# Kernel optimization log

Hardware: AMD Instinct MI355X
Metric: run time of the kernel (lower is better)

## Reference

```python
import jax, jax.numpy as jnp
import numpy as np

# Config constants (match init_kwargs)
T = 1024            # num_tokens
H = 2048            # hidden_size
E = 16              # n_routed_experts
I = 1408            # moe_intermediate_size
TOP_K = 4           # num_experts_per_tok
N_GROUP = 4         # n_group
TOPK_GROUP = 2      # topk_group
N_SHARED = 2        # n_shared_experts
SI = I * N_SHARED   # shared intermediate = 2816
ROUTED_SCALE = 1.0  # routed_scaling_factor
RENORMALIZE = True  # norm_topk_prob


def setup_inputs() -> dict:
    key = jax.random.key(0)
    ks = jax.random.split(key, 6)
    scale_w = 0.02  # keep router logits in a sane range
    return {
        "x": jax.random.normal(ks[0], (T, H), dtype=jnp.float32),
        "gate_w": jax.random.normal(ks[1], (E, H), dtype=jnp.float32) * scale_w,
        "w_gate_up": jax.random.normal(ks[2], (E, H, 2 * I), dtype=jnp.float32) * scale_w,
        "w_down": jax.random.normal(ks[3], (E, I, H), dtype=jnp.float32) * scale_w,
        "shared_gate_up": jax.random.normal(ks[4], (H, 2 * SI), dtype=jnp.float32) * scale_w,
        "shared_down": jax.random.normal(ks[5], (SI, H), dtype=jnp.float32) * scale_w,
    }


def _silu_and_mul(gu):
    gate, up = jnp.split(gu, 2, axis=-1)
    return jax.nn.silu(gate) * up


def _grouped_topk(logits):
    # scores over experts, grouped top-k group selection, then top-k experts
    scores = jax.nn.softmax(logits, axis=-1)                          # [T, E]
    group_scores = scores.reshape(T, N_GROUP, E // N_GROUP).max(-1)   # [T, G]
    _, grp_idx = jax.lax.top_k(group_scores, TOPK_GROUP)              # [T, topk_group]
    grp_mask = jnp.zeros((T, N_GROUP), scores.dtype).at[
        jnp.arange(T)[:, None], grp_idx].set(1.0)                     # [T, G]
    score_mask = jnp.repeat(grp_mask, E // N_GROUP, axis=1)           # [T, E]
    tmp = jnp.where(score_mask > 0, scores, 0.0)
    topk_w, topk_ids = jax.lax.top_k(tmp, TOP_K)                      # [T, K]
    if RENORMALIZE:
        topk_w = topk_w / jnp.sum(topk_w, axis=-1, keepdims=True)
    # dense combine-weight matrix [T, E] (top-k ids are distinct per token)
    cw = jnp.zeros((T, E), scores.dtype).at[
        jnp.arange(T)[:, None], topk_ids].set(topk_w)
    return cw


def reference(x, gate_w, w_gate_up, w_down, shared_gate_up, shared_down):
    # shared experts MLP (SiluAndMul)
    shared_out = _silu_and_mul(x @ shared_gate_up) @ shared_down      # [T, H]

    # router
    logits = x @ gate_w.T                                             # [T, E]
    cw = _grouped_topk(logits)                                        # [T, E]

    # routed experts: dense grouped GEMM over all experts, masked combine
    h = jnp.einsum('th,ehi->eti', x, w_gate_up)                       # [E, T, 2I]
    a = _silu_and_mul(h)                                              # [E, T, I]
    y = jnp.einsum('eti,eih->eth', a, w_down)                         # [E, T, H]
    routed = jnp.einsum('eth,te->th', y, cw)                          # [T, H]

    return routed * ROUTED_SCALE + shared_out
```

## Files before the change

kernel.cpp:

```cpp
#include <hip/hip_runtime.h>
#include <hip/hip_bf16.h>
#include <stdint.h>
#include <math.h>

#define T_TOK 1024
#define H_DIM 2048
#define E_NUM 16
#define I_DIM 1408
#define TOPK  4
#define SI_DIM 2816
#define NSLOT (T_TOK * TOPK)

typedef short bf16x8 __attribute__((ext_vector_type(8)));
typedef float f32x4  __attribute__((ext_vector_type(4)));

__device__ __forceinline__ uint32_t fbf(float f) {
  __hip_bfloat16 h = __float2bfloat16(f);
  return (uint32_t)*reinterpret_cast<uint16_t*>(&h);
}
__device__ __forceinline__ float asf(uint32_t u) {
  union { uint32_t u; float f; } c; c.u = u; return c.f;
}

typedef const __attribute__((address_space(1))) char gld_g;
typedef __attribute__((address_space(3))) char gld_l;
__device__ __forceinline__ void gload16(const void* g, void* l) {
  __builtin_amdgcn_global_load_lds((gld_g*)g, (gld_l*)l, 16, 0, 0);
}
__device__ __forceinline__ void barrier_lgkm() {
  asm volatile("s_waitcnt lgkmcnt(0)" ::: "memory");
  __builtin_amdgcn_s_barrier();
  __builtin_amdgcn_sched_barrier(0);
}

__global__ __launch_bounds__(256) void k_router(const float* __restrict__ x,
                                                const float* __restrict__ gw,
                                                int* __restrict__ topk_id,
                                                float* __restrict__ topk_w) {
  int t = blockIdx.x;
  float acc[E_NUM];
#pragma unroll
  for (int e = 0; e < E_NUM; ++e) acc[e] = 0.f;
  for (int h = threadIdx.x; h < H_DIM; h += 256) {
    float xv = x[(long)t * H_DIM + h];
#pragma unroll
    for (int e = 0; e < E_NUM; ++e) acc[e] += xv * gw[e * H_DIM + h];
  }
#pragma unroll
  for (int e = 0; e < E_NUM; ++e) {
#pragma unroll
    for (int off = 32; off; off >>= 1) acc[e] += __shfl_down(acc[e], off);
  }
  __shared__ float part[4][E_NUM];
  int wid = threadIdx.x >> 6, lane = threadIdx.x & 63;
  if (lane == 0) {
#pragma unroll
    for (int e = 0; e < E_NUM; ++e) part[wid][e] = acc[e];
  }
  __syncthreads();
  if (threadIdx.x == 0) {
    float lg[E_NUM], p[E_NUM];
    float m = -1e30f;
    for (int e = 0; e < E_NUM; ++e) {
      lg[e] = part[0][e] + part[1][e] + part[2][e] + part[3][e];
      m = fmaxf(m, lg[e]);
    }
    float s = 0.f;
    for (int e = 0; e < E_NUM; ++e) { p[e] = expf(lg[e] - m); s += p[e]; }
    float inv = 1.f / s;
    for (int e = 0; e < E_NUM; ++e) p[e] *= inv;
    float gs[4];
    for (int g = 0; g < 4; ++g) {
      float mg = p[g * 4];
      for (int i = 1; i < 4; ++i) mg = fmaxf(mg, p[g * 4 + i]);
      gs[g] = mg;
    }
    int g1 = 0;
    for (int g = 1; g < 4; ++g) if (gs[g] > gs[g1]) g1 = g;
    int g2 = -1;
    for (int g = 0; g < 4; ++g) {
      if (g == g1) continue;
      if (g2 < 0 || gs[g] > gs[g2]) g2 = g;
    }
    float q[E_NUM];
    for (int e = 0; e < E_NUM; ++e)
      q[e] = ((e >> 2) == g1 || (e >> 2) == g2) ? p[e] : -1e30f;
    int ids[TOPK]; float wv[TOPK]; float wsum = 0.f;
    for (int k = 0; k < TOPK; ++k) {
      int best = 0; float bv = -2e30f;
      for (int e = 0; e < E_NUM; ++e) if (q[e] > bv) { bv = q[e]; best = e; }
      ids[k] = best; wv[k] = p[best]; wsum += p[best]; q[best] = -3e30f;
    }
    float winv = 1.f / wsum;
    for (int k = 0; k < TOPK; ++k) {
      topk_id[t * TOPK + k] = ids[k];
      topk_w[t * TOPK + k] = wv[k] * winv;
    }
  }
}

__global__ __launch_bounds__(256) void k_count(const int* __restrict__ topk_id,
                                               int* __restrict__ counts) {
  int e = blockIdx.x, tid = threadIdx.x;
  int c = 0;
  for (int s = tid; s < NSLOT; s += 256) c += (topk_id[s] == e);
#pragma unroll
  for (int off = 32; off; off >>= 1) c += __shfl_down(c, off);
  __shared__ int wsum[4];
  int wid = tid >> 6, lane = tid & 63;
  if (lane == 0) wsum[wid] = c;
  __syncthreads();
  if (tid == 0) counts[e] = wsum[0] + wsum[1] + wsum[2] + wsum[3];
}

__global__ void k_offs(const int* __restrict__ counts, int* __restrict__ offs,
                       int* __restrict__ cum) {
  if (threadIdx.x == 0 && blockIdx.x == 0) {
    int s = 0, c = 0;
    cum[0] = 0;
    for (int e = 0; e < E_NUM; ++e) {
      offs[e] = s; s += counts[e];
      c += (counts[e] + 255) >> 8;
      cum[e + 1] = c;
    }
    offs[E_NUM] = s;
  }
}

__global__ __launch_bounds__(256) void k_fill(const int* __restrict__ topk_id,
                                              const int* __restrict__ offs,
                                              int* __restrict__ tok_of_row,
                                              int* __restrict__ row_of_slot) {
  int e = blockIdx.x, tid = threadIdx.x;
  int t0 = tid * 4;
  int match[4]; int cnt = 0;
#pragma unroll
  for (int i = 0; i < 4; ++i) {
    int t = t0 + i; int mk = -1;
#pragma unroll
    for (int k = 0; k < TOPK; ++k) if (topk_id[t * TOPK + k] == e) mk = k;
    match[i] = mk; cnt += (mk >= 0);
  }
  __shared__ int sc[256];
  sc[tid] = cnt; __syncthreads();
  for (int d = 1; d < 256; d <<= 1) {
    int v = sc[tid];
    if (tid >= d) v += sc[tid - d];
    __syncthreads();
    sc[tid] = v;
    __syncthreads();
  }
  int row = offs[e] + sc[tid] - cnt;
#pragma unroll
  for (int i = 0; i < 4; ++i) {
    if (match[i] >= 0) {
      tok_of_row[row] = t0 + i;
      row_of_slot[(t0 + i) * TOPK + match[i]] = row;
      ++row;
    }
  }
}

__global__ __launch_bounds__(256) void k_cvt(const float* __restrict__ in,
                                             uint16_t* __restrict__ out) {
  int i = (blockIdx.x * 256 + threadIdx.x) * 4;
  float4 v = *(const float4*)(in + i);
  uint2 p;
  p.x = fbf(v.x) | (fbf(v.y) << 16);
  p.y = fbf(v.z) | (fbf(v.w) << 16);
  *(uint2*)(out + i) = p;
}

template <int MODE>
__global__ __launch_bounds__(256, 2) void k_gemm(
    const uint16_t* __restrict__ As, int ldas,
    const float* __restrict__ Bs, int ldbs, int upS,
    void* __restrict__ OutS, int ldoS, int NMs, int NNs, int Ks, int f32S,
    const uint16_t* __restrict__ Ar, int ldar,
    const float* __restrict__ Br, int ldbr, long bstr, int upR,
    void* __restrict__ OutR, int ldoR, int NN1, int K1, int f32R,
    const int* __restrict__ offs, const int* __restrict__ rowlist,
    const int* __restrict__ cum) {
  constexpr int BN = (MODE == 0) ? 64 : 128;
  constexpr int NI = (MODE == 0) ? 2 : 4;
  constexpr int BB = 32768;
  constexpr int BMS = 5120;
  __shared__ char smem[43008];

  const int S = NMs * NNs;
  const int NBw = S + cum[E_NUM] * NN1;
  int f = blockIdx.x;
  if (f >= NBw) return;
  int q = NBw >> 3, r = NBw & 7;
  int xcd = f & 7, o = f >> 3;
  int f2 = (xcd < r ? xcd * (q + 1) : r * (q + 1) + (xcd - r) * q) + o;

  const uint16_t* A; const float* Bp; void* Outp; const int* rl;
  int lda, ldb, up, ldo, K, m0, n0, row_end, isf32;
  if (f2 < S) {
    int mb = f2 % NMs, nb = f2 / NMs;
    A = As; lda = ldas; Bp = Bs; ldb = ldbs; up = upS;
    Outp = OutS; ldo = ldoS; K = Ks; isf32 = f32S; rl = nullptr;
    m0 = mb * 256; row_end = NMs * 256; n0 = nb * BN;
  } else {
    int g = f2 - S;
    int e = 0;
    for (e = 0; e < E_NUM; ++e) if (g < cum[e + 1] * NN1) break;
    if (e == E_NUM) return;
    int nmbe = cum[e + 1] - cum[e];
    int loc = g - cum[e] * NN1;
    int mb = loc % nmbe, nb = loc / nmbe;
    A = Ar; lda = ldar; Bp = Br + (size_t)e * bstr; ldb = ldbr; up = upR;
    Outp = OutR; ldo = ldoR; K = K1; isf32 = f32R; rl = rowlist;
    m0 = offs[e] + mb * 256; row_end = offs[e + 1]; n0 = nb * BN;
  }

  const int tid = threadIdx.x;
  const int wid = tid >> 6, lane = tid & 63;
  const int wm = (wid >> 1) * 64, wn = (wid & 1) * (BN / 2);
  const int lrow = lane & 15, kg = lane >> 4;

  const uint16_t* aSrc[4]; int aDst[4];
#pragma unroll
  for (int p = 0; p < 4; ++p) {
    int rr = wid * 64 + p * 16 + (lane >> 2);
    int grow = m0 + rr;
    grow = grow < row_end - 1 ? grow : row_end - 1;
    int arow = rl ? rl[grow] : grow;
    int sslot = (lane & 3) ^ ((lane >> 3) & 3);
    aSrc[p] = A + (size_t)arow * lda + sslot * 8;
    aDst[p] = wid * 4096 + p * 1024;
  }

  int n4, kq, mat;
  if constexpr (MODE == 0) {
    n4 = (tid & 15) * 4; int rest = tid >> 4; kq = rest & 7; mat = rest >> 3;
  } else {
    n4 = (tid & 31) * 4; kq = tid >> 5; mat = 0;
  }
  const int k0 = kq * 4;
  const float* bptr = Bp + (size_t)k0 * ldb + n0 + n4 + (mat ? up : 0);
  const int sq = (kq >> 1) & 3, hf = kq & 1;
  int bw[4];
#pragma unroll
  for (int j = 0; j < 4; ++j) {
    int n = n4 + j;
    bw[j] = BB + mat * BMS + n * 80 + ((sq ^ ((n >> 4) & 3)) << 4) + (hf << 3);
  }

  float4 v[4];
  auto loadB = [&]() {
#pragma unroll
    for (int i = 0; i < 4; ++i) v[i] = *(const float4*)(bptr + (size_t)i * ldb);
    bptr += (size_t)32 * ldb;
  };
  auto stageB = [&]() {
#pragma unroll
    for (int j = 0; j < 4; ++j) {
      uint2 w;
      w.x = fbf(((const float*)&v[0])[j]) | (fbf(((const float*)&v[1])[j]) << 16);
      w.y = fbf(((const float*)&v[2])[j]) | (fbf(((const float*)&v[3])[j]) << 16);
      *(uint2*)(smem + bw[j]) = w;
    }
  };

  f32x4 zero = {0.f, 0.f, 0.f, 0.f};
  f32x4 accg[2][4][NI];
  f32x4 accu[(MODE == 0) ? 2 : 1][(MODE == 0) ? 4 : 1][(MODE == 0) ? NI : 1];
#pragma unroll
  for (int mt = 0; mt < 2; ++mt)
#pragma unroll
    for (int mi = 0; mi < 4; ++mi)
#pragma unroll
      for (int ni = 0; ni < NI; ++ni) {
        accg[mt][mi][ni] = zero;
        if constexpr (MODE == 0) accu[mt][mi][ni] = zero;
      }

  auto compute = [&](int cur) {
    const char* ab = smem + cur * 16384;
    const int akx = (kg ^ ((lrow >> 1) & 3)) << 4;
    bf16x8 af[8];
#pragma unroll
    for (int mt = 0; mt < 2; ++mt)
#pragma unroll
      for (int mi = 0; mi < 4; ++mi) {
        int row = mt * 128 + wm + mi * 16 + lrow;
        af[mt * 4 + mi] = *(const bf16x8*)(ab + row * 64 + akx);
      }
#pragma unroll
    for (int ni = 0; ni < NI; ++ni) {
      int n = wn + ni * 16 + lrow;
      int bo = BB + n * 80 + ((kg ^ ((n >> 4) & 3)) << 4);
      bf16x8 bg = *(const bf16x8*)(smem + bo);
#pragma unroll
      for (int mt = 0; mt < 2; ++mt)
#pragma unroll
        for (int mi = 0; mi < 4; ++mi)
          accg[mt][mi][ni] = __builtin_amdgcn_mfma_f32_16x16x32_bf16(
              af[mt * 4 + mi], bg, accg[mt][mi][ni], 0, 0, 0);
      if constexpr (MODE == 0) {
        bf16x8 bu = *(const bf16x8*)(smem + bo + BMS);
#pragma unroll
        for (int mt = 0; mt < 2; ++mt)
#pragma unroll
          for (int mi = 0; mi < 4; ++mi)
            accu[mt][mi][ni] = __builtin_amdgcn_mfma_f32_16x16x32_bf16(
                af[mt * 4 + mi], bu, accu[mt][mi][ni], 0, 0, 0);
      }
    }
  };

  const int nk = K >> 5;
#pragma unroll
  for (int p = 0; p < 4; ++p) { gload16(aSrc[p], smem + aDst[p]); aSrc[p] += 32; }
  loadB();

  for (int kt = 0; kt < nk; ++kt) {
    const int cur = kt & 1;
    __syncthreads();
    if (kt + 1 < nk) {
#pragma unroll
      for (int p = 0; p < 4; ++p) {
        gload16(aSrc[p], smem + (cur ^ 1) * 16384 + aDst[p]); aSrc[p] += 32;
      }
    }
    stageB();
    if (kt + 1 < nk) loadB();
    barrier_lgkm();
    compute(cur);
  }

#pragma unroll
  for (int mt = 0; mt < 2; ++mt) {
#pragma unroll
    for (int mi = 0; mi < 4; ++mi) {
#pragma unroll
      for (int rr = 0; rr < 4; ++rr) {
        int grow = m0 + mt * 128 + wm + mi * 16 + kg * 4 + rr;
        if (grow >= row_end) continue;
#pragma unroll
        for (int ni = 0; ni < NI; ++ni) {
          int col = n0 + wn + ni * 16 + lrow;
          float g = accg[mt][mi][ni][rr];
          if constexpr (MODE == 0) {
            float u = accu[mt][mi][ni][rr];
            float a = g / (1.f + __expf(-g)) * u;
            ((uint16_t*)Outp)[(size_t)grow * ldo + col] = (uint16_t)fbf(a);
          } else {
            if (isf32)
              ((float*)Outp)[(size_t)grow * ldo + col] = g;
            else
              ((uint16_t*)Outp)[(size_t)grow * ldo + col] = (uint16_t)fbf(g);
          }
        }
      }
    }
  }
}

__global__ __launch_bounds__(256) void k_combine(float* __restrict__ out,
    const uint16_t* __restrict__ y, const int* __restrict__ row_of_slot,
    const float* __restrict__ topk_w, const float* __restrict__ p0) {
  int t = blockIdx.x, tid = threadIdx.x;
  int h = tid * 8;
  size_t off = (size_t)t * H_DIM + h;
  float4 o0 = *(const float4*)(p0 + off);
  float4 o1 = *(const float4*)(p0 + off + 4);
#pragma unroll
  for (int k = 0; k < TOPK; ++k) {
    int row = row_of_slot[t * TOPK + k];
    float wk = topk_w[t * TOPK + k];
    uint4 v = *(const uint4*)(y + (size_t)row * H_DIM + h);
    o0.x += wk * asf(v.x << 16); o0.y += wk * asf(v.x & 0xffff0000u);
    o0.z += wk * asf(v.y << 16); o0.w += wk * asf(v.y & 0xffff0000u);
    o1.x += wk * asf(v.z << 16); o1.y += wk * asf(v.z & 0xffff0000u);
    o1.z += wk * asf(v.w << 16); o1.w += wk * asf(v.w & 0xffff0000u);
  }
  *(float4*)(out + off) = o0;
  *(float4*)(out + off + 4) = o1;
}

extern "C" void kernel_launch(void* const* d_in, const int* in_sizes, int n_in,
                              void* d_out, int out_size, void* d_ws,
                              size_t ws_size, hipStream_t stream) {
  const float* x   = (const float*)d_in[0];
  const float* gw  = (const float*)d_in[1];
  const float* wgu = (const float*)d_in[2];
  const float* wd  = (const float*)d_in[3];
  const float* sgu = (const float*)d_in[4];
  const float* sd  = (const float*)d_in[5];
  float* out = (float*)d_out;

  char* ws = (char*)d_ws;
  int*   topk_id     = (int*)(ws + 0);
  float* topk_w      = (float*)(ws + 16384);
  int*   counts      = (int*)(ws + 32768);
  int*   offs        = (int*)(ws + 33792);
  int*   cum         = (int*)(ws + 34816);
  int*   tok_of_row  = (int*)(ws + 35840);
  int*   row_of_slot = (int*)(ws + 52224);
  uint16_t* x_bf     = (uint16_t*)(ws + 131072);
  uint16_t* act      = (uint16_t*)(ws + 4325376);
  uint16_t* yslots   = (uint16_t*)(ws + 15859712);
  uint16_t* act_sh   = (uint16_t*)(ws + 32636928);
  bool merged = ws_size >= (size_t)38404096 + 8388608;
  float* p0 = merged ? (float*)(ws + 38404096) : (float*)(ws + 4325376);

  k_router<<<T_TOK, 256, 0, stream>>>(x, gw, topk_id, topk_w);
  k_count<<<E_NUM, 256, 0, stream>>>(topk_id, counts);
  k_offs<<<1, 1, 0, stream>>>(counts, offs, cum);
  k_fill<<<E_NUM, 256, 0, stream>>>(topk_id, offs, tok_of_row, row_of_slot);
  k_cvt<<<(T_TOK * H_DIM) / 1024, 256, 0, stream>>>(x, x_bf);

  k_gemm<0><<<176 + 32 * 22, 256, 0, stream>>>(
      x_bf, H_DIM, sgu, 2 * SI_DIM, SI_DIM, act_sh, SI_DIM, 4, 44, H_DIM, 0,
      x_bf, H_DIM, wgu, 2 * I_DIM, (long)H_DIM * 2 * I_DIM, I_DIM,
      act, I_DIM, 22, H_DIM, 0,
      offs, tok_of_row, cum);

  if (merged) {
    k_gemm<1><<<64 + 32 * 16, 256, 0, stream>>>(
        act_sh, SI_DIM, sd, H_DIM, 0, p0, H_DIM, 4, 16, SI_DIM, 1,
        act, I_DIM, wd, H_DIM, (long)I_DIM * H_DIM, 0,
        yslots, H_DIM, 16, I_DIM, 0,
        offs, nullptr, cum);
  } else {
    k_gemm<1><<<32 * 16, 256, 0, stream>>>(
        act_sh, SI_DIM, sd, H_DIM, 0, p0, H_DIM, 4, 0, SI_DIM, 1,
        act, I_DIM, wd, H_DIM, (long)I_DIM * H_DIM, 0,
        yslots, H_DIM, 16, I_DIM, 0,
        offs, nullptr, cum);
    k_gemm<1><<<64, 256, 0, stream>>>(
        act_sh, SI_DIM, sd, H_DIM, 0, p0, H_DIM, 4, 16, SI_DIM, 1,
        act, I_DIM, wd, H_DIM, (long)I_DIM * H_DIM, 0,
        yslots, H_DIM, 0, I_DIM, 0,
        offs, nullptr, cum);
  }
  k_combine<<<T_TOK, 256, 0, stream>>>(out, yslots, row_of_slot, topk_w, p0);
}
```

Baseline: 322.1 us.

## Stream fp32 B tiles directly into LDS and convert to bf16 at fragment read

Replaces the register-staged B path (global float4 loads, bf16 packing, LDS store) with asynchronous global_load_lds copies of raw fp32 B tiles into a double-buffered, XOR-swizzled LDS region. Each MFMA B fragment is now assembled from eight scalar fp32 LDS reads converted to bf16 inside the compute loop. The goal is to remove staging registers and the extra barrier so B loads overlap compute like the A loads already do. In exchange, LDS use grows to 64KB per block, LDS read traffic roughly doubles, and every wave repeats the fp32-to-bf16 conversion on the MFMA critical path.

```diff
diff --git a/kernel.cpp b/kernel.cpp
--- a/kernel.cpp
+++ b/kernel.cpp
@@ -26,11 +26,6 @@
 typedef __attribute__((address_space(3))) char gld_l;
 __device__ __forceinline__ void gload16(const void* g, void* l) {
   __builtin_amdgcn_global_load_lds((gld_g*)g, (gld_l*)l, 16, 0, 0);
-}
-__device__ __forceinline__ void barrier_lgkm() {
-  asm volatile("s_waitcnt lgkmcnt(0)" ::: "memory");
-  __builtin_amdgcn_s_barrier();
-  __builtin_amdgcn_sched_barrier(0);
 }
 
 __global__ __launch_bounds__(256) void k_router(const float* __restrict__ x,
@@ -183,9 +178,9 @@
     const int* __restrict__ cum) {
   constexpr int BN = (MODE == 0) ? 64 : 128;
   constexpr int NI = (MODE == 0) ? 2 : 4;
-  constexpr int BB = 32768;
-  constexpr int BMS = 5120;
-  __shared__ char smem[43008];
+  constexpr int ROWB = BN * 4;
+  constexpr int MATS = (MODE == 0) ? 8192 : 0;
+  __shared__ char smem[65536];
 
   const int S = NMs * NNs;
   const int NBw = S + cum[E_NUM] * NN1;
@@ -231,36 +226,39 @@
     aSrc[p] = A + (size_t)arow * lda + sslot * 8;
     aDst[p] = wid * 4096 + p * 1024;
   }
-
-  int n4, kq, mat;
-  if constexpr (MODE == 0) {
-    n4 = (tid & 15) * 4; int rest = tid >> 4; kq = rest & 7; mat = rest >> 3;
-  } else {
-    n4 = (tid & 31) * 4; kq = tid >> 5; mat = 0;
-  }
-  const int k0 = kq * 4;
-  const float* bptr = Bp + (size_t)k0 * ldb + n0 + n4 + (mat ? up : 0);
-  const int sq = (kq >> 1) & 3, hf = kq & 1;
-  int bw[4];
-#pragma unroll
-  for (int j = 0; j < 4; ++j) {
-    int n = n4 + j;
-    bw[j] = BB + mat * BMS + n * 80 + ((sq ^ ((n >> 4) & 3)) << 4) + (hf << 3);
-  }
-
-  float4 v[4];
-  auto loadB = [&]() {
-#pragma unroll
-    for (int i = 0; i < 4; ++i) v[i] = *(const float4*)(bptr + (size_t)i * ldb);
-    bptr += (size_t)32 * ldb;
+  auto issueA = [&](int buf) {
+#pragma unroll
+    for (int p = 0; p < 4; ++p) {
+      gload16(aSrc[p], smem + buf * 16384 + aDst[p]);
+      aSrc[p] += 32;
+    }
   };
-  auto stageB = [&]() {
-#pragma unroll
-    for (int j = 0; j < 4; ++j) {
-      uint2 w;
-      w.x = fbf(((const float*)&v[0])[j]) | (fbf(((const float*)&v[1])[j]) << 16);
-      w.y = fbf(((const float*)&v[2])[j]) | (fbf(((const float*)&v[3])[j]) << 16);
-      *(uint2*)(smem + bw[j]) = w;
+
+  const float* bSrc[4]; int bDst[4];
+#pragma unroll
+  for (int p = 0; p < 4; ++p) {
+    int i = wid * 4 + p;
+    int kk, sl, base;
+    if constexpr (MODE == 0) {
+      int mat = i >> 3, k4 = (i & 7) * 4;
+      kk = k4 + (lane >> 4); sl = lane & 15;
+      base = 32768 + mat * MATS + k4 * ROWB;
+      bSrc[p] = Bp + (size_t)kk * ldb + n0 + (mat ? up : 0) +
+                ((sl ^ (((kk >> 3) & 1) << 2)) * 4);
+    } else {
+      int k2 = i * 2;
+      kk = k2 + (lane >> 5); sl = lane & 31;
+      base = 32768 + k2 * ROWB;
+      bSrc[p] = Bp + (size_t)kk * ldb + n0 +
+                ((sl ^ (((kk >> 3) & 1) << 2)) * 4);
+    }
+    bDst[p] = base;
+  }
+  auto issueB = [&](int buf) {
+#pragma unroll
+    for (int p = 0; p < 4; ++p) {
+      gload16(bSrc[p], smem + buf * 16384 + bDst[p]);
+      bSrc[p] += (size_t)32 * ldb;
     }
   };
 
@@ -279,6 +277,7 @@
 
   auto compute = [&](int cur) {
     const char* ab = smem + cur * 16384;
+    const char* bb = smem + 32768 + cur * 16384;
     const int akx = (kg ^ ((lrow >> 1) & 3)) << 4;
     bf16x8 af[8];
 #pragma unroll
@@ -288,11 +287,15 @@
         int row = mt * 128 + wm + mi * 16 + lrow;
         af[mt * 4 + mi] = *(const bf16x8*)(ab + row * 64 + akx);
       }
+    const char* rowbase = bb + (kg * 8) * ROWB;
 #pragma unroll
     for (int ni = 0; ni < NI; ++ni) {
       int n = wn + ni * 16 + lrow;
-      int bo = BB + n * 80 + ((kg ^ ((n >> 4) & 3)) << 4);
-      bf16x8 bg = *(const bf16x8*)(smem + bo);
+      int sX = ((n >> 2) ^ ((kg & 1) << 2)) * 16 + (n & 3) * 4;
+      bf16x8 bg;
+#pragma unroll
+      for (int j = 0; j < 8; ++j)
+        bg[j] = (short)fbf(*(const float*)(rowbase + j * ROWB + sX));
 #pragma unroll
       for (int mt = 0; mt < 2; ++mt)
 #pragma unroll
@@ -300,7 +303,10 @@
           accg[mt][mi][ni] = __builtin_amdgcn_mfma_f32_16x16x32_bf16(
               af[mt * 4 + mi], bg, accg[mt][mi][ni], 0, 0, 0);
       if constexpr (MODE == 0) {
-        bf16x8 bu = *(const bf16x8*)(smem + bo + BMS);
+        bf16x8 bu;
+#pragma unroll
+        for (int j = 0; j < 8; ++j)
+          bu[j] = (short)fbf(*(const float*)(rowbase + MATS + j * ROWB + sX));
 #pragma unroll
         for (int mt = 0; mt < 2; ++mt)
 #pragma unroll
@@ -312,22 +318,11 @@
   };
 
   const int nk = K >> 5;
-#pragma unroll
-  for (int p = 0; p < 4; ++p) { gload16(aSrc[p], smem + aDst[p]); aSrc[p] += 32; }
-  loadB();
-
+  issueA(0); issueB(0);
   for (int kt = 0; kt < nk; ++kt) {
     const int cur = kt & 1;
     __syncthreads();
-    if (kt + 1 < nk) {
-#pragma unroll
-      for (int p = 0; p < 4; ++p) {
-        gload16(aSrc[p], smem + (cur ^ 1) * 16384 + aDst[p]); aSrc[p] += 32;
-      }
-    }
-    stageB();
-    if (kt + 1 < nk) loadB();
-    barrier_lgkm();
+    if (kt + 1 < nk) { issueA(cur ^ 1); issueB(cur ^ 1); }
     compute(cur);
   }
 
```

Result: slower. 337.4 us (+4.7%).

## Fuse routing prep kernels and stream fp32 gate-up weights via async LDS loads

Applied to the files above, without the earlier changes.

Folds the bf16 conversion of x and the expert counting (now done with atomics) into the router kernel. Offset and cumulative-block computation moves into k_fill, which removes the separate count, offsets and convert launches. The gate/up GEMM is split into its own kernel that copies fp32 weight tiles straight into a larger double-buffered LDS with global_load_lds, then converts them to bf16 at MFMA time. This drops the register-staged B path, at the cost of more LDS (64KB), per-element conversion inside the inner loop, and an extra memset.

```diff
diff --git a/kernel.cpp b/kernel.cpp
--- a/kernel.cpp
+++ b/kernel.cpp
@@ -36,8 +36,21 @@
 __global__ __launch_bounds__(256) void k_router(const float* __restrict__ x,
                                                 const float* __restrict__ gw,
                                                 int* __restrict__ topk_id,
-                                                float* __restrict__ topk_w) {
+                                                float* __restrict__ topk_w,
+                                                int* __restrict__ counts,
+                                                uint16_t* __restrict__ x_bf) {
   int t = blockIdx.x;
+  {
+    const float4* xin = (const float4*)(x + (size_t)t * H_DIM);
+    uint16_t* xb = x_bf + (size_t)t * H_DIM;
+    for (int i = threadIdx.x; i < H_DIM / 4; i += 256) {
+      float4 v = xin[i];
+      uint2 pck;
+      pck.x = fbf(v.x) | (fbf(v.y) << 16);
+      pck.y = fbf(v.z) | (fbf(v.w) << 16);
+      *(uint2*)(xb + i * 4) = pck;
+    }
+  }
   float acc[E_NUM];
 #pragma unroll
   for (int e = 0; e < E_NUM; ++e) acc[e] = 0.f;
@@ -95,43 +108,34 @@
     for (int k = 0; k < TOPK; ++k) {
       topk_id[t * TOPK + k] = ids[k];
       topk_w[t * TOPK + k] = wv[k] * winv;
-    }
-  }
-}
-
-__global__ __launch_bounds__(256) void k_count(const int* __restrict__ topk_id,
-                                               int* __restrict__ counts) {
-  int e = blockIdx.x, tid = threadIdx.x;
-  int c = 0;
-  for (int s = tid; s < NSLOT; s += 256) c += (topk_id[s] == e);
-#pragma unroll
-  for (int off = 32; off; off >>= 1) c += __shfl_down(c, off);
-  __shared__ int wsum[4];
-  int wid = tid >> 6, lane = tid & 63;
-  if (lane == 0) wsum[wid] = c;
-  __syncthreads();
-  if (tid == 0) counts[e] = wsum[0] + wsum[1] + wsum[2] + wsum[3];
-}
-
-__global__ void k_offs(const int* __restrict__ counts, int* __restrict__ offs,
-                       int* __restrict__ cum) {
-  if (threadIdx.x == 0 && blockIdx.x == 0) {
-    int s = 0, c = 0;
-    cum[0] = 0;
-    for (int e = 0; e < E_NUM; ++e) {
-      offs[e] = s; s += counts[e];
-      c += (counts[e] + 255) >> 8;
-      cum[e + 1] = c;
-    }
-    offs[E_NUM] = s;
+      atomicAdd(&counts[ids[k]], 1);
+    }
   }
 }
 
 __global__ __launch_bounds__(256) void k_fill(const int* __restrict__ topk_id,
-                                              const int* __restrict__ offs,
+                                              const int* __restrict__ counts,
+                                              int* __restrict__ offs,
+                                              int* __restrict__ cum,
                                               int* __restrict__ tok_of_row,
                                               int* __restrict__ row_of_slot) {
   int e = blockIdx.x, tid = threadIdx.x;
+  __shared__ int base_s;
+  if (tid == 0) {
+    int s = 0;
+    for (int j = 0; j < e; ++j) s += counts[j];
+    base_s = s;
+    if (e == 0) {
+      int ss = 0, c = 0;
+      cum[0] = 0;
+      for (int j = 0; j < E_NUM; ++j) {
+        offs[j] = ss; ss += counts[j];
+        c += (counts[j] + 255) >> 8;
+        cum[j + 1] = c;
+      }
+      offs[E_NUM] = ss;
+    }
+  }
   int t0 = tid * 4;
   int match[4]; int cnt = 0;
 #pragma unroll
@@ -150,7 +154,7 @@
     sc[tid] = v;
     __syncthreads();
   }
-  int row = offs[e] + sc[tid] - cnt;
+  int row = base_s + sc[tid] - cnt;
 #pragma unroll
   for (int i = 0; i < 4; ++i) {
     if (match[i] >= 0) {
@@ -161,31 +165,20 @@
   }
 }
 
-__global__ __launch_bounds__(256) void k_cvt(const float* __restrict__ in,
-                                             uint16_t* __restrict__ out) {
-  int i = (blockIdx.x * 256 + threadIdx.x) * 4;
-  float4 v = *(const float4*)(in + i);
-  uint2 p;
-  p.x = fbf(v.x) | (fbf(v.y) << 16);
-  p.y = fbf(v.z) | (fbf(v.w) << 16);
-  *(uint2*)(out + i) = p;
-}
-
-template <int MODE>
-__global__ __launch_bounds__(256, 2) void k_gemm(
+__global__ __launch_bounds__(256, 2) void k_gemm0(
     const uint16_t* __restrict__ As, int ldas,
     const float* __restrict__ Bs, int ldbs, int upS,
-    void* __restrict__ OutS, int ldoS, int NMs, int NNs, int Ks, int f32S,
+    void* __restrict__ OutS, int ldoS, int NMs, int NNs, int Ks,
     const uint16_t* __restrict__ Ar, int ldar,
     const float* __restrict__ Br, int ldbr, long bstr, int upR,
-    void* __restrict__ OutR, int ldoR, int NN1, int K1, int f32R,
+    void* __restrict__ OutR, int ldoR, int NN1, int K1,
     const int* __restrict__ offs, const int* __restrict__ rowlist,
     const int* __restrict__ cum) {
-  constexpr int BN = (MODE == 0) ? 64 : 128;
-  constexpr int NI = (MODE == 0) ? 2 : 4;
-  constexpr int BB = 32768;
-  constexpr int BMS = 5120;
-  __shared__ char smem[43008];
+  constexpr int BN = 64;
+  constexpr int NI = 2;
+  constexpr int ROWB = BN * 4;
+  constexpr int MATS = 8192;
+  __shared__ char smem[65536];
 
   const int S = NMs * NNs;
   const int NBw = S + cum[E_NUM] * NN1;
@@ -196,11 +189,11 @@
   int f2 = (xcd < r ? xcd * (q + 1) : r * (q + 1) + (xcd - r) * q) + o;
 
   const uint16_t* A; const float* Bp; void* Outp; const int* rl;
-  int lda, ldb, up, ldo, K, m0, n0, row_end, isf32;
+  int lda, ldb, up, ldo, K, m0, n0, row_end;
   if (f2 < S) {
     int mb = f2 % NMs, nb = f2 / NMs;
     A = As; lda = ldas; Bp = Bs; ldb = ldbs; up = upS;
-    Outp = OutS; ldo = ldoS; K = Ks; isf32 = f32S; rl = nullptr;
+    Outp = OutS; ldo = ldoS; K = Ks; rl = nullptr;
     m0 = mb * 256; row_end = NMs * 256; n0 = nb * BN;
   } else {
     int g = f2 - S;
@@ -211,7 +204,7 @@
     int loc = g - cum[e] * NN1;
     int mb = loc % nmbe, nb = loc / nmbe;
     A = Ar; lda = ldar; Bp = Br + (size_t)e * bstr; ldb = ldbr; up = upR;
-    Outp = OutR; ldo = ldoR; K = K1; isf32 = f32R; rl = rowlist;
+    Outp = OutR; ldo = ldoR; K = K1; rl = rowlist;
     m0 = offs[e] + mb * 256; row_end = offs[e + 1]; n0 = nb * BN;
   }
 
@@ -231,21 +224,179 @@
     aSrc[p] = A + (size_t)arow * lda + sslot * 8;
     aDst[p] = wid * 4096 + p * 1024;
   }
-
-  int n4, kq, mat;
-  if constexpr (MODE == 0) {
-    n4 = (tid & 15) * 4; int rest = tid >> 4; kq = rest & 7; mat = rest >> 3;
+  auto issueA = [&](int buf) {
+#pragma unroll
+    for (int p = 0; p < 4; ++p) {
+      gload16(aSrc[p], smem + buf * 16384 + aDst[p]);
+      aSrc[p] += 32;
+    }
+  };
+
+  const float* bSrc[4]; int bDst[4];
+#pragma unroll
+  for (int p = 0; p < 4; ++p) {
+    int i = wid * 4 + p;
+    int mat = i >> 3, k4 = (i & 7) * 4;
+    int kk = k4 + (lane >> 4);
+    int sl = lane & 15;
+    bSrc[p] = Bp + (size_t)kk * ldb + n0 + (mat ? up : 0) +
+              ((sl ^ (((kk >> 3) & 1) << 2)) * 4);
+    bDst[p] = 32768 + mat * MATS + k4 * ROWB;
+  }
+  auto issueB = [&](int buf) {
+#pragma unroll
+    for (int p = 0; p < 4; ++p) {
+      gload16(bSrc[p], smem + buf * 16384 + bDst[p]);
+      bSrc[p] += (size_t)32 * ldb;
+    }
+  };
+
+  f32x4 zero = {0.f, 0.f, 0.f, 0.f};
+  f32x4 accg[2][4][NI], accu[2][4][NI];
+#pragma unroll
+  for (int mt = 0; mt < 2; ++mt)
+#pragma unroll
+    for (int mi = 0; mi < 4; ++mi)
+#pragma unroll
+      for (int ni = 0; ni < NI; ++ni) { accg[mt][mi][ni] = zero; accu[mt][mi][ni] = zero; }
+
+  auto compute = [&](int cur) {
+    const char* ab = smem + cur * 16384;
+    const char* bb = smem + 32768 + cur * 16384;
+    const int akx = (kg ^ ((lrow >> 1) & 3)) << 4;
+    bf16x8 af[8];
+#pragma unroll
+    for (int mt = 0; mt < 2; ++mt)
+#pragma unroll
+      for (int mi = 0; mi < 4; ++mi) {
+        int row = mt * 128 + wm + mi * 16 + lrow;
+        af[mt * 4 + mi] = *(const bf16x8*)(ab + row * 64 + akx);
+      }
+    const char* rowbase = bb + (kg * 8) * ROWB;
+#pragma unroll
+    for (int ni = 0; ni < NI; ++ni) {
+      int n = wn + ni * 16 + lrow;
+      int sX = ((n >> 2) ^ ((kg & 1) << 2)) * 16 + (n & 3) * 4;
+      bf16x8 bg;
+#pragma unroll
+      for (int j = 0; j < 8; ++j)
+        bg[j] = (short)fbf(*(const float*)(rowbase + j * ROWB + sX));
+#pragma unroll
+      for (int mt = 0; mt < 2; ++mt)
+#pragma unroll
+        for (int mi = 0; mi < 4; ++mi)
+          accg[mt][mi][ni] = __builtin_amdgcn_mfma_f32_16x16x32_bf16(
+              af[mt * 4 + mi], bg, accg[mt][mi][ni], 0, 0, 0);
+      bf16x8 bu;
+#pragma unroll
+      for (int j = 0; j < 8; ++j)
+        bu[j] = (short)fbf(*(const float*)(rowbase + MATS + j * ROWB + sX));
+#pragma unroll
+      for (int mt = 0; mt < 2; ++mt)
+#pragma unroll
+        for (int mi = 0; mi < 4; ++mi)
+          accu[mt][mi][ni] = __builtin_amdgcn_mfma_f32_16x16x32_bf16(
+              af[mt * 4 + mi], bu, accu[mt][mi][ni], 0, 0, 0);
+    }
+  };
+
+  const int nk = K >> 5;
+  issueA(0); issueB(0);
+  for (int kt = 0; kt < nk; ++kt) {
+    const int cur = kt & 1;
+    __syncthreads();
+    if (kt + 1 < nk) { issueA(cur ^ 1); issueB(cur ^ 1); }
+    compute(cur);
+  }
+
+#pragma unroll
+  for (int mt = 0; mt < 2; ++mt) {
+#pragma unroll
+    for (int mi = 0; mi < 4; ++mi) {
+#pragma unroll
+      for (int rr = 0; rr < 4; ++rr) {
+        int grow = m0 + mt * 128 + wm + mi * 16 + kg * 4 + rr;
+        if (grow >= row_end) continue;
+#pragma unroll
+        for (int ni = 0; ni < NI; ++ni) {
+          int col = n0 + wn + ni * 16 + lrow;
+          float g = accg[mt][mi][ni][rr];
+          float u = accu[mt][mi][ni][rr];
+          float a = g / (1.f + __expf(-g)) * u;
+          ((uint16_t*)Outp)[(size_t)grow * ldo + col] = (uint16_t)fbf(a);
+        }
+      }
+    }
+  }
+}
+
+__global__ __launch_bounds__(256, 2) void k_gemm1(
+    const uint16_t* __restrict__ As, int ldas,
+    const float* __restrict__ Bs, int ldbs,
+    void* __restrict__ OutS, int ldoS, int NMs, int NNs, int Ks, int f32S,
+    const uint16_t* __restrict__ Ar, int ldar,
+    const float* __restrict__ Br, int ldbr, long bstr,
+    void* __restrict__ OutR, int ldoR, int NN1, int K1, int f32R,
+    const int* __restrict__ offs, const int* __restrict__ cum) {
+  constexpr int BN = 128;
+  constexpr int NI = 4;
+  constexpr int BB = 32768;
+  __shared__ char smem[43008];
+
+  const int S = NMs * NNs;
+  const int NBw = S + cum[E_NUM] * NN1;
+  int f = blockIdx.x;
+  if (f >= NBw) return;
+  int q = NBw >> 3, r = NBw & 7;
+  int xcd = f & 7, o = f >> 3;
+  int f2 = (xcd < r ? xcd * (q + 1) : r * (q + 1) + (xcd - r) * q) + o;
+
+  const uint16_t* A; const float* Bp; void* Outp;
+  int lda, ldb, ldo, K, m0, n0, row_end, isf32;
+  if (f2 < S) {
+    int mb = f2 % NMs, nb = f2 / NMs;
+    A = As; lda = ldas; Bp = Bs; ldb = ldbs;
+    Outp = OutS; ldo = ldoS; K = Ks; isf32 = f32S;
+    m0 = mb * 256; row_end = NMs * 256; n0 = nb * BN;
   } else {
-    n4 = (tid & 31) * 4; kq = tid >> 5; mat = 0;
-  }
+    int g = f2 - S;
+    int e = 0;
+    for (e = 0; e < E_NUM; ++e) if (g < cum[e + 1] * NN1) break;
+    if (e == E_NUM) return;
+    int nmbe = cum[e + 1] - cum[e];
+    int loc = g - cum[e] * NN1;
+    int mb = loc % nmbe, nb = loc / nmbe;
+    A = Ar; lda = ldar; Bp = Br + (size_t)e * bstr; ldb = ldbr;
+    Outp = OutR; ldo = ldoR; K = K1; isf32 = f32R;
+    m0 = offs[e] + mb * 256; row_end = offs[e + 1]; n0 = nb * BN;
+  }
+
+  const int tid = threadIdx.x;
+  const int wid = tid >> 6, lane = tid & 63;
+  const int wm = (wid >> 1) * 64, wn = (wid & 1) * 64;
+  const int lrow = lane & 15, kg = lane >> 4;
+
+  const uint16_t* aSrc[4]; int aDst[4];
+#pragma unroll
+  for (int p = 0; p < 4; ++p) {
+    int rr = wid * 64 + p * 16 + (lane >> 2);
+    int grow = m0 + rr;
+    grow = grow < row_end - 1 ? grow : row_end - 1;
+    int sslot = (lane & 3) ^ ((lane >> 3) & 3);
+    aSrc[p] = A + (size_t)grow * lda + sslot * 8;
+    aDst[p] = wid * 4096 + p * 1024;
+  }
+
+  const int n4 = (tid & 31) * 4;
+  const int kq = tid >> 5;
   const int k0 = kq * 4;
-  const float* bptr = Bp + (size_t)k0 * ldb + n0 + n4 + (mat ? up : 0);
+  const float* bptr = Bp + (size_t)k0 * ldb + n0 + n4;
   const int sq = (kq >> 1) & 3, hf = kq & 1;
   int bw[4];
 #pragma unroll
   for (int j = 0; j < 4; ++j) {
     int n = n4 + j;
-    bw[j] = BB + mat * BMS + n * 80 + ((sq ^ ((n >> 4) & 3)) << 4) + (hf << 3);
+    bw[j] = BB + n * 80 + ((sq ^ ((n >> 4) & 3)) << 4) + (hf << 3);
   }
 
   float4 v[4];
@@ -266,16 +417,12 @@
 
   f32x4 zero = {0.f, 0.f, 0.f, 0.f};
   f32x4 accg[2][4][NI];
-  f32x4 accu[(MODE == 0) ? 2 : 1][(MODE == 0) ? 4 : 1][(MODE == 0) ? NI : 1];
 #pragma unroll
   for (int mt = 0; mt < 2; ++mt)
 #pragma unroll
     for (int mi = 0; mi < 4; ++mi)
 #pragma unroll
-      for (int ni = 0; ni < NI; ++ni) {
-        accg[mt][mi][ni] = zero;
-        if constexpr (MODE == 0) accu[mt][mi][ni] = zero;
-      }
+      for (int ni = 0; ni < NI; ++ni) accg[mt][mi][ni] = zero;
 
   auto compute = [&](int cur) {
     const char* ab = smem + cur * 16384;
@@ -299,15 +446,6 @@
         for (int mi = 0; mi < 4; ++mi)
           accg[mt][mi][ni] = __builtin_amdgcn_mfma_f32_16x16x32_bf16(
               af[mt * 4 + mi], bg, accg[mt][mi][ni], 0, 0, 0);
-      if constexpr (MODE == 0) {
-        bf16x8 bu = *(const bf16x8*)(smem + bo + BMS);
-#pragma unroll
-        for (int mt = 0; mt < 2; ++mt)
-#pragma unroll
-          for (int mi = 0; mi < 4; ++mi)
-            accu[mt][mi][ni] = __builtin_amdgcn_mfma_f32_16x16x32_bf16(
-                af[mt * 4 + mi], bu, accu[mt][mi][ni], 0, 0, 0);
-      }
     }
   };
 
@@ -343,16 +481,10 @@
         for (int ni = 0; ni < NI; ++ni) {
           int col = n0 + wn + ni * 16 + lrow;
           float g = accg[mt][mi][ni][rr];
-          if constexpr (MODE == 0) {
-            float u = accu[mt][mi][ni][rr];
-            float a = g / (1.f + __expf(-g)) * u;
-            ((uint16_t*)Outp)[(size_t)grow * ldo + col] = (uint16_t)fbf(a);
-          } else {
-            if (isf32)
-              ((float*)Outp)[(size_t)grow * ldo + col] = g;
-            else
-              ((uint16_t*)Outp)[(size_t)grow * ldo + col] = (uint16_t)fbf(g);
-          }
+          if (isf32)
+            ((float*)Outp)[(size_t)grow * ldo + col] = g;
+          else
+            ((uint16_t*)Outp)[(size_t)grow * ldo + col] = (uint16_t)fbf(g);
         }
       }
     }
@@ -407,35 +539,34 @@
   bool merged = ws_size >= (size_t)38404096 + 8388608;
   float* p0 = merged ? (float*)(ws + 38404096) : (float*)(ws + 4325376);
 
-  k_router<<<T_TOK, 256, 0, stream>>>(x, gw, topk_id, topk_w);
-  k_count<<<E_NUM, 256, 0, stream>>>(topk_id, counts);
-  k_offs<<<1, 1, 0, stream>>>(counts, offs, cum);
-  k_fill<<<E_NUM, 256, 0, stream>>>(topk_id, offs, tok_of_row, row_of_slot);
-  k_cvt<<<(T_TOK * H_DIM) / 1024, 256, 0, stream>>>(x, x_bf);
-
-  k_gemm<0><<<176 + 32 * 22, 256, 0, stream>>>(
-      x_bf, H_DIM, sgu, 2 * SI_DIM, SI_DIM, act_sh, SI_DIM, 4, 44, H_DIM, 0,
+  hipMemsetAsync(counts, 0, E_NUM * sizeof(int), stream);
+  k_router<<<T_TOK, 256, 0, stream>>>(x, gw, topk_id, topk_w, counts, x_bf);
+  k_fill<<<E_NUM, 256, 0, stream>>>(topk_id, counts, offs, cum,
+                                    tok_of_row, row_of_slot);
+
+  k_gemm0<<<176 + 32 * 22, 256, 0, stream>>>(
+      x_bf, H_DIM, sgu, 2 * SI_DIM, SI_DIM, act_sh, SI_DIM, 4, 44, H_DIM,
       x_bf, H_DIM, wgu, 2 * I_DIM, (long)H_DIM * 2 * I_DIM, I_DIM,
-      act, I_DIM, 22, H_DIM, 0,
+      act, I_DIM, 22, H_DIM,
       offs, tok_of_row, cum);
 
   if (merged) {
-    k_gemm<1><<<64 + 32 * 16, 256, 0, stream>>>(
-        act_sh, SI_DIM, sd, H_DIM, 0, p0, H_DIM, 4, 16, SI_DIM, 1,
-        act, I_DIM, wd, H_DIM, (long)I_DIM * H_DIM, 0,
+    k_gemm1<<<64 + 32 * 16, 256, 0, stream>>>(
+        act_sh, SI_DIM, sd, H_DIM, p0, H_DIM, 4, 16, SI_DIM, 1,
+        act, I_DIM, wd, H_DIM, (long)I_DIM * H_DIM,
         yslots, H_DIM, 16, I_DIM, 0,
-        offs, nullptr, cum);
+        offs, cum);
   } else {
-    k_gemm<1><<<32 * 16, 256, 0, stream>>>(
-        act_sh, SI_DIM, sd, H_DIM, 0, p0, H_DIM, 4, 0, SI_DIM, 1,
-        act, I_DIM, wd, H_DIM, (long)I_DIM * H_DIM, 0,
+    k_gemm1<<<32 * 16, 256, 0, stream>>>(
+        act_sh, SI_DIM, sd, H_DIM, p0, H_DIM, 4, 0, SI_DIM, 1,
+        act, I_DIM, wd, H_DIM, (long)I_DIM * H_DIM,
         yslots, H_DIM, 16, I_DIM, 0,
-        offs, nullptr, cum);
-    k_gemm<1><<<64, 256, 0, stream>>>(
-        act_sh, SI_DIM, sd, H_DIM, 0, p0, H_DIM, 4, 16, SI_DIM, 1,
-        act, I_DIM, wd, H_DIM, (long)I_DIM * H_DIM, 0,
+        offs, cum);
+    k_gemm1<<<64, 256, 0, stream>>>(
+        act_sh, SI_DIM, sd, H_DIM, p0, H_DIM, 4, 16, SI_DIM, 1,
+        act, I_DIM, wd, H_DIM, (long)I_DIM * H_DIM,
         yslots, H_DIM, 0, I_DIM, 0,
-        offs, nullptr, cum);
+        offs, cum);
   }
   k_combine<<<T_TOK, 256, 0, stream>>>(out, yslots, row_of_slot, topk_w, p0);
 }
```

After: 362.8 us. 1.13x slower.

## Double-buffer B tile in LDS and drop second barrier per k-step

Applied to the files above, without the earlier changes.

Adds a second LDS buffer for the converted B tile and keeps two register sets of prefetched B values. The k-loop is unrolled by two so each step needs only one barrier, with the next tile's A global-to-LDS loads and B stores overlapping the current MFMA compute. The goal is to remove the extra lgkm wait and barrier that previously sat between staging and compute. The cost is more LDS (53 KB vs 43 KB), which may limit occupancy, plus extra registers. It relies on the single __syncthreads to order the async global_load_lds writes before they are read, which is a correctness risk.

```diff
diff --git a/kernel.cpp b/kernel.cpp
--- a/kernel.cpp
+++ b/kernel.cpp
@@ -26,11 +26,6 @@
 typedef __attribute__((address_space(3))) char gld_l;
 __device__ __forceinline__ void gload16(const void* g, void* l) {
   __builtin_amdgcn_global_load_lds((gld_g*)g, (gld_l*)l, 16, 0, 0);
-}
-__device__ __forceinline__ void barrier_lgkm() {
-  asm volatile("s_waitcnt lgkmcnt(0)" ::: "memory");
-  __builtin_amdgcn_s_barrier();
-  __builtin_amdgcn_sched_barrier(0);
 }
 
 __global__ __launch_bounds__(256) void k_router(const float* __restrict__ x,
@@ -184,8 +179,9 @@
   constexpr int BN = (MODE == 0) ? 64 : 128;
   constexpr int NI = (MODE == 0) ? 2 : 4;
   constexpr int BB = 32768;
+  constexpr int BBUF = 10240;
   constexpr int BMS = 5120;
-  __shared__ char smem[43008];
+  __shared__ char smem[53248];
 
   const int S = NMs * NNs;
   const int NBw = S + cum[E_NUM] * NN1;
@@ -231,6 +227,13 @@
     aSrc[p] = A + (size_t)arow * lda + sslot * 8;
     aDst[p] = wid * 4096 + p * 1024;
   }
+  auto issueA = [&](int buf) {
+#pragma unroll
+    for (int p = 0; p < 4; ++p) {
+      gload16(aSrc[p], smem + buf * 16384 + aDst[p]);
+      aSrc[p] += 32;
+    }
+  };
 
   int n4, kq, mat;
   if constexpr (MODE == 0) {
@@ -245,22 +248,23 @@
 #pragma unroll
   for (int j = 0; j < 4; ++j) {
     int n = n4 + j;
-    bw[j] = BB + mat * BMS + n * 80 + ((sq ^ ((n >> 4) & 3)) << 4) + (hf << 3);
-  }
-
-  float4 v[4];
-  auto loadB = [&]() {
+    bw[j] = mat * BMS + n * 80 + ((sq ^ ((n >> 4) & 3)) << 4) + (hf << 3);
+  }
+
+  float4 vA[4], vB[4];
+  auto loadB = [&](float4 (&v)[4]) {
 #pragma unroll
     for (int i = 0; i < 4; ++i) v[i] = *(const float4*)(bptr + (size_t)i * ldb);
     bptr += (size_t)32 * ldb;
   };
-  auto stageB = [&]() {
+  auto stageB = [&](int buf, const float4 (&v)[4]) {
+    char* bb = smem + BB + buf * BBUF;
 #pragma unroll
     for (int j = 0; j < 4; ++j) {
       uint2 w;
       w.x = fbf(((const float*)&v[0])[j]) | (fbf(((const float*)&v[1])[j]) << 16);
       w.y = fbf(((const float*)&v[2])[j]) | (fbf(((const float*)&v[3])[j]) << 16);
-      *(uint2*)(smem + bw[j]) = w;
+      *(uint2*)(bb + bw[j]) = w;
     }
   };
 
@@ -279,6 +283,7 @@
 
   auto compute = [&](int cur) {
     const char* ab = smem + cur * 16384;
+    const char* bb = smem + BB + cur * BBUF;
     const int akx = (kg ^ ((lrow >> 1) & 3)) << 4;
     bf16x8 af[8];
 #pragma unroll
@@ -291,8 +296,8 @@
 #pragma unroll
     for (int ni = 0; ni < NI; ++ni) {
       int n = wn + ni * 16 + lrow;
-      int bo = BB + n * 80 + ((kg ^ ((n >> 4) & 3)) << 4);
-      bf16x8 bg = *(const bf16x8*)(smem + bo);
+      int bo = n * 80 + ((kg ^ ((n >> 4) & 3)) << 4);
+      bf16x8 bg = *(const bf16x8*)(bb + bo);
 #pragma unroll
       for (int mt = 0; mt < 2; ++mt)
 #pragma unroll
@@ -300,7 +305,7 @@
           accg[mt][mi][ni] = __builtin_amdgcn_mfma_f32_16x16x32_bf16(
               af[mt * 4 + mi], bg, accg[mt][mi][ni], 0, 0, 0);
       if constexpr (MODE == 0) {
-        bf16x8 bu = *(const bf16x8*)(smem + bo + BMS);
+        bf16x8 bu = *(const bf16x8*)(bb + bo + BMS);
 #pragma unroll
         for (int mt = 0; mt < 2; ++mt)
 #pragma unroll
@@ -312,23 +317,22 @@
   };
 
   const int nk = K >> 5;
-#pragma unroll
-  for (int p = 0; p < 4; ++p) { gload16(aSrc[p], smem + aDst[p]); aSrc[p] += 32; }
-  loadB();
-
-  for (int kt = 0; kt < nk; ++kt) {
-    const int cur = kt & 1;
+  loadB(vA);
+  issueA(0);
+  stageB(0, vA);
+  loadB(vB);
+
+  for (int kt = 0; kt < nk; kt += 2) {
     __syncthreads();
+    if (kt + 1 < nk) { issueA(1); stageB(1, vB); }
+    if (kt + 2 < nk) loadB(vA);
+    compute(0);
     if (kt + 1 < nk) {
-#pragma unroll
-      for (int p = 0; p < 4; ++p) {
-        gload16(aSrc[p], smem + (cur ^ 1) * 16384 + aDst[p]); aSrc[p] += 32;
-      }
-    }
-    stageB();
-    if (kt + 1 < nk) loadB();
-    barrier_lgkm();
-    compute(cur);
+      __syncthreads();
+      if (kt + 2 < nk) { issueA(0); stageB(0, vA); }
+      if (kt + 3 < nk) loadB(vB);
+      compute(1);
+    }
   }
 
 #pragma unroll
```

Result: slower. 388.4 us (+20.6%).
